# Kernel tuning notes

Measured on AMD Instinct MI355X. Metric: run time of the kernel, lower is better.

## Reference

```python
import jax, jax.numpy as jnp
import numpy as np

NLAT, NLON = 64, 64
CIN = 512
HEADS = 8


def _cc_weights(n):
    # Clenshaw-Curtis quadrature weights on [-1, 1] for nodes cos(k*pi/(n-1)),
    # as used by torch-harmonics for the 'equiangular' grid. Weights sum to 2.
    N = n - 1
    theta = np.pi * np.arange(n) / N
    m = N // 2
    j = np.arange(1, m + 1)
    b = np.where(2 * j == N, 1.0, 2.0)
    S = (b / (4.0 * j ** 2 - 1.0))[None, :] * np.cos(2.0 * j[None, :] * theta[:, None])
    w = 1.0 - S.sum(axis=1)
    c = np.full(n, 2.0)
    c[0] = 1.0
    c[-1] = 1.0
    return c * w / N


def _log_quad_weights(nlat, nlon):
    # _precompute_latitudes flips nodes/weights; then 2*pi*w/nlon tiled over lon.
    w = _cc_weights(nlat)[::-1].copy()
    qw = 2.0 * np.pi * w / nlon                       # (nlat,)
    qw = np.tile(qw[:, None], (1, nlon)).reshape(-1)  # (nlat*nlon,)
    return jnp.asarray(np.log(qw), dtype=jnp.float32)


def setup_inputs() -> dict:
    key = jax.random.key(0)
    ks = jax.random.split(key, 5)
    s_qkv = float(np.sqrt(3.0 / CIN))   # scale for q/k/v 1x1-conv weights
    s_proj = float(np.sqrt(3.0 / CIN))  # out_channels == CIN
    u = lambda k, sh, s: jax.random.uniform(k, sh, jnp.float32, -s, s)
    return dict(
        query=jax.random.normal(ks[0], (1, CIN, NLAT, NLON), jnp.float32),
        q_w=u(ks[1], (CIN, CIN), s_qkv), q_b=jnp.zeros((CIN,), jnp.float32),
        k_w=u(ks[2], (CIN, CIN), s_qkv), k_b=jnp.zeros((CIN,), jnp.float32),
        v_w=u(ks[3], (CIN, CIN), s_qkv), v_b=jnp.zeros((CIN,), jnp.float32),
        p_w=u(ks[4], (CIN, CIN), s_proj), p_b=jnp.zeros((CIN,), jnp.float32),
        log_quad_weights=_log_quad_weights(NLAT, NLON),
    )


def reference(query, q_w, q_b, k_w, k_b, v_w, v_b, p_w, p_b, log_quad_weights):
    B, C, H, W = query.shape
    hd = C // HEADS  # head dim (k_channels == out_channels == in_channels)

    def proj_tokens(x, w, b):
        # 1x1 conv == channel matmul, then split heads and flatten H*W tokens
        y = jnp.einsum('bihw,oi->bohw', x, w) + b[None, :, None, None]
        return y.reshape(B, HEADS, -1, H, W).transpose(0, 1, 3, 4, 2).reshape(B, HEADS, H * W, -1)

    q = proj_tokens(query, q_w, q_b)  # (B, heads, HW, hd)
    k = proj_tokens(query, k_w, k_b)  # self-attention: key/value default to query
    v = proj_tokens(query, v_w, v_b)

    scale = 1.0 / jnp.sqrt(jnp.asarray(hd, dtype=q.dtype))
    # additive log-quadrature bias over keys (broadcast over batch/head/query)
    logits = jnp.einsum('bhqd,bhkd->bhqk', q, k) * scale + log_quad_weights[None, None, None, :]
    attn = jax.nn.softmax(logits, axis=-1)
    out = jnp.einsum('bhqk,bhkd->bhqd', attn, v)          # (B, heads, HW, hd)
    out = out.transpose(0, 1, 3, 2).reshape(B, HEADS * hd, H, W)
    return jnp.einsum('bihw,oi->bohw', out, p_w) + p_b[None, :, None, None]
```

## Files before the change

### kernel.cpp

```cpp
#include <hip/hip_runtime.h>

typedef unsigned short u16;
typedef unsigned int u32;
typedef __bf16 bf16x8 __attribute__((ext_vector_type(8)));
typedef float f32x4 __attribute__((ext_vector_type(4)));
typedef unsigned short u16x4 __attribute__((ext_vector_type(4)));

#define LOG2E 1.4426950408889634f

#if __has_builtin(__builtin_amdgcn_exp2f)
#define EXP2F(x) __builtin_amdgcn_exp2f(x)
#else
#define EXP2F(x) exp2f(x)
#endif

__device__ __forceinline__ u16 f2bf(float f) {
    union { float f; u32 u; } a; a.f = f;
    u32 u = a.u;
    u += 0x7FFFu + ((u >> 16) & 1u);
    return (u16)(u >> 16);
}
__device__ __forceinline__ bf16x8 ldg8(const u16* p) {
    return *reinterpret_cast<const bf16x8*>(p);
}
#if __has_builtin(__builtin_amdgcn_cvt_pk_bf16_f32)
__device__ __forceinline__ u32 pack2(float a, float b) {
    auto r = __builtin_amdgcn_cvt_pk_bf16_f32(a, b);
    return __builtin_bit_cast(u32, r);
}
#else
__device__ __forceinline__ u32 pack2(float a, float b) {
    u32 ua = __float_as_uint(a) + 0x8000u;
    u32 ub = __float_as_uint(b) + 0x8000u;
    return __builtin_amdgcn_perm(ub, ua, 0x07060302);
}
#endif
__device__ __forceinline__ void async16(const void* g, void* l) {
    __builtin_amdgcn_global_load_lds(
        (const __attribute__((address_space(1))) u32*)g,
        (__attribute__((address_space(3))) u32*)l, 16, 0, 0);
}

#define MFMA16(a, b, c) __builtin_amdgcn_mfma_f32_16x16x32_bf16((a), (b), (c), 0, 0, 0)

__global__ __launch_bounds__(256) void prep(const float* __restrict__ X,
                                            u16* __restrict__ Xt,
                                            const float* __restrict__ s0,
                                            const float* __restrict__ s1,
                                            const float* __restrict__ s2,
                                            const float* __restrict__ s3,
                                            u16* __restrict__ Wqkv,
                                            u16* __restrict__ Wp,
                                            const float* __restrict__ lqw,
                                            float* __restrict__ lqw2g) {
    __shared__ u16 tile[64][65];
    const int tid = threadIdx.x;
    const int y = blockIdx.y;

    if (y < 8) {
        const int t0 = blockIdx.x * 64;
        const int c0 = y * 64;
#pragma unroll
        for (int i = 0; i < 16; ++i) {
            int idx = tid + i * 256;
            int r = idx >> 6, cc = idx & 63;
            tile[r][cc] = f2bf(X[(size_t)(c0 + r) * 4096 + t0 + cc]);
        }
        __syncthreads();
#pragma unroll
        for (int i = 0; i < 16; ++i) {
            int idx = tid + i * 256;
            int tr = idx >> 6, cc = idx & 63;
            Xt[(size_t)(t0 + tr) * 512 + c0 + cc] = tile[cc][tr];
        }
    } else if (y < 12) {
        const int m = y - 8;
        const float* s = (m == 0) ? s0 : (m == 1) ? s1 : (m == 2) ? s2 : s3;
        u16* d = (m == 3) ? Wp : Wqkv + (size_t)m * 262144;
#pragma unroll
        for (int j = 0; j < 4; ++j) {
            int i = blockIdx.x * 1024 + j * 256 + tid;
            float4 v = reinterpret_cast<const float4*>(s)[i];
            u16x4 o;
            o[0] = f2bf(v.x); o[1] = f2bf(v.y); o[2] = f2bf(v.z); o[3] = f2bf(v.w);
            reinterpret_cast<u16x4*>(d)[i] = o;
        }
    } else {
        if (blockIdx.x < 4) {
            int i = blockIdx.x * 256 + tid;
            float4 v = reinterpret_cast<const float4*>(lqw)[i];
            v.x *= LOG2E; v.y *= LOG2E; v.z *= LOG2E; v.w *= LOG2E;
            reinterpret_cast<float4*>(lqw2g)[i] = v;
        }
    }
}

__global__ __launch_bounds__(512, 2) void qkv_gemm(const u16* __restrict__ Wqkv,
                                                   const u16* __restrict__ Xt,
                                                   const float* __restrict__ qb,
                                                   const float* __restrict__ kb,
                                                   const float* __restrict__ vb,
                                                   u16* __restrict__ Qt,
                                                   u16* __restrict__ Kt,
                                                   u16* __restrict__ Vp) {
    __shared__ __align__(16) u16 Al[2][128 * 32];
    __shared__ __align__(16) u16 Bl[2][128 * 32];

    const int tid = threadIdx.x;
    const int w = tid >> 6, lane = tid & 63;
    const int quad = lane >> 4, lm = lane & 15;
    const int wm = w & 1, wn = w >> 1;
    const int n0 = blockIdx.x * 128;
    const int my = blockIdx.y;
    const int m0 = my * 128;

    const int arow = lane >> 2;
    const int sch = (lane & 3) ^ ((lane >> 3) & 3);
    const u16* agp = Wqkv + (size_t)(m0 + w * 16 + arow) * 512 + sch * 8;
    const u16* bgp = Xt + (size_t)(n0 + w * 16 + arow) * 512 + sch * 8;

    async16(agp, &Al[0][w * 16 * 32]);
    async16(bgp, &Bl[0][w * 16 * 32]);
    agp += 32; bgp += 32;

    const int FOFF = lm * 64 + ((quad ^ ((lm >> 1) & 3)) << 4);

    f32x4 acc[4][2];
#pragma unroll
    for (int mt = 0; mt < 4; ++mt)
#pragma unroll
        for (int bt = 0; bt < 2; ++bt) acc[mt][bt] = (f32x4){0.f, 0.f, 0.f, 0.f};

    __syncthreads();

    for (int s = 0; s < 16; ++s) {
        const int buf = s & 1;
        if (s < 15) {
            async16(agp, &Al[buf ^ 1][w * 16 * 32]);
            async16(bgp, &Bl[buf ^ 1][w * 16 * 32]);
            agp += 32; bgp += 32;
        }
        const char* Ab = (const char*)&Al[buf][0];
        const char* Bb = (const char*)&Bl[buf][0];
        bf16x8 af[4], bfr[2];
#pragma unroll
        for (int mt = 0; mt < 4; ++mt)
            af[mt] = *(const bf16x8*)(Ab + wm * 4096 + mt * 1024 + FOFF);
#pragma unroll
        for (int bt = 0; bt < 2; ++bt)
            bfr[bt] = *(const bf16x8*)(Bb + wn * 2048 + bt * 1024 + FOFF);
#pragma unroll
        for (int mt = 0; mt < 4; ++mt)
#pragma unroll
            for (int bt = 0; bt < 2; ++bt)
                acc[mt][bt] = MFMA16(af[mt], bfr[bt], acc[mt][bt]);
        __syncthreads();
    }

    const int mat = my >> 2;
    const float* bias = (mat == 0) ? qb : (mat == 1) ? kb : vb;
    const int chbase = (my & 3) * 128 + wm * 64 + quad * 4;

    if (mat < 2) {
        u16* out = mat ? Kt : Qt;
        const float sc = mat ? 1.0f : 0.125f * LOG2E;
#pragma unroll
        for (int mt = 0; mt < 4; ++mt) {
            const int ch = chbase + mt * 16;
            float4 bv = *(const float4*)(bias + ch);
            float bvf[4] = {bv.x, bv.y, bv.z, bv.w};
#pragma unroll
            for (int bt = 0; bt < 2; ++bt) {
                int tok = n0 + wn * 32 + bt * 16 + lm;
                u16x4 pk;
#pragma unroll
                for (int r = 0; r < 4; ++r)
                    pk[r] = f2bf((acc[mt][bt][r] + bvf[r]) * sc);
                *(u16x4*)(out + (size_t)tok * 512 + ch) = pk;
            }
        }
    } else {
#pragma unroll
        for (int mt = 0; mt < 4; ++mt) {
            const int ch = chbase + mt * 16;
            float4 bv = *(const float4*)(bias + ch);
            float bvf[4] = {bv.x, bv.y, bv.z, bv.w};
#pragma unroll
            for (int bt = 0; bt < 2; ++bt) {
                int g = bt * 16 + lm;
                int col = n0 + wn * 32 + 8 * ((g >> 2) & 3) + 4 * ((g >> 4) & 1) + (g & 3);
#pragma unroll
                for (int r = 0; r < 4; ++r)
                    Vp[(size_t)(ch + r) * 4096 + col] = f2bf(acc[mt][bt][r] + bvf[r]);
            }
        }
    }
}

__global__ __launch_bounds__(256, 2) void out_gemm(const u16* __restrict__ Wp,
                                                   const u16* __restrict__ Ot,
                                                   const float* __restrict__ pb,
                                                   float* __restrict__ out) {
    __shared__ __align__(16) u16 Al[2][128 * 32];
    __shared__ __align__(16) u16 Bl[2][64 * 32];

    const int tid = threadIdx.x;
    const int w = tid >> 6, lane = tid & 63;
    const int quad = lane >> 4, lm = lane & 15;
    const int wm = w & 1, wn = w >> 1;
    const int n0 = blockIdx.x * 64;
    const int m0 = blockIdx.y * 128;

    const int arow = lane >> 2;
    const int sch = (lane & 3) ^ ((lane >> 3) & 3);
    const u16* agp0 = Wp + (size_t)(m0 + w * 16 + arow) * 512 + sch * 8;
    const u16* agp1 = agp0 + (size_t)64 * 512;
    const u16* bgp = Ot + (size_t)(n0 + w * 16 + arow) * 512 + sch * 8;

    async16(agp0, &Al[0][w * 16 * 32]);
    async16(agp1, &Al[0][(64 + w * 16) * 32]);
    async16(bgp, &Bl[0][w * 16 * 32]);
    agp0 += 32; agp1 += 32; bgp += 32;

    const int FOFF = lm * 64 + ((quad ^ ((lm >> 1) & 3)) << 4);

    f32x4 acc[4][2];
#pragma unroll
    for (int mt = 0; mt < 4; ++mt)
#pragma unroll
        for (int bt = 0; bt < 2; ++bt) acc[mt][bt] = (f32x4){0.f, 0.f, 0.f, 0.f};

    __syncthreads();

    for (int s = 0; s < 16; ++s) {
        const int buf = s & 1;
        if (s < 15) {
            async16(agp0, &Al[buf ^ 1][w * 16 * 32]);
            async16(agp1, &Al[buf ^ 1][(64 + w * 16) * 32]);
            async16(bgp, &Bl[buf ^ 1][w * 16 * 32]);
            agp0 += 32; agp1 += 32; bgp += 32;
        }
        const char* Ab = (const char*)&Al[buf][0];
        const char* Bb = (const char*)&Bl[buf][0];
        bf16x8 af[4], bfr[2];
#pragma unroll
        for (int mt = 0; mt < 4; ++mt)
            af[mt] = *(const bf16x8*)(Ab + wm * 4096 + mt * 1024 + FOFF);
#pragma unroll
        for (int bt = 0; bt < 2; ++bt)
            bfr[bt] = *(const bf16x8*)(Bb + wn * 2048 + bt * 1024 + FOFF);
#pragma unroll
        for (int mt = 0; mt < 4; ++mt)
#pragma unroll
            for (int bt = 0; bt < 2; ++bt)
                acc[mt][bt] = MFMA16(af[mt], bfr[bt], acc[mt][bt]);
        __syncthreads();
    }

#pragma unroll
    for (int mt = 0; mt < 4; ++mt) {
        const int ch = m0 + wm * 64 + mt * 16 + quad * 4;
        float4 bv = *(const float4*)(pb + ch);
        float bvf[4] = {bv.x, bv.y, bv.z, bv.w};
#pragma unroll
        for (int bt = 0; bt < 2; ++bt) {
            int tok = n0 + wn * 32 + bt * 16 + lm;
#pragma unroll
            for (int r = 0; r < 4; ++r)
                out[(size_t)(ch + r) * 4096 + tok] = acc[mt][bt][r] + bvf[r];
        }
    }
}

__global__ __launch_bounds__(512, 2) void flash_attn(const u16* __restrict__ Qt,
                                                     const u16* __restrict__ Kt,
                                                     const u16* __restrict__ Vp,
                                                     const float* __restrict__ lqw2g,
                                                     u16* __restrict__ Ot) {
    __shared__ __align__(16) u16 kv[2][2][2][4096];

    const int tid = threadIdx.x;
    const int w = tid >> 6, lane = tid & 63;
    const int quad = lane >> 4, lm = lane & 15;
    const int qw = w & 3, half = w >> 2;
    const int h = blockIdx.y, hq = h * 64;
    const int q0 = blockIdx.x * 64 + qw * 16;
    const int kstart = half * 2048;

    char* kvb = (char*)&kv[0][0][0][0] + half * 32768;
    const int srow = lane >> 3;
    const int schunk = (lane & 7) ^ srow;
    const u16* kgp = Kt + (size_t)(kstart + qw * 16 + srow) * 512 + hq + schunk * 8;
    const u16* kgp8 = kgp + (size_t)8 * 512;
    const u16* vgp = Vp + (size_t)(hq + qw * 16 + srow) * 4096 + kstart + schunk * 8;
    const u16* vgp8 = vgp + (size_t)8 * 4096;

    {
        char* nb = kvb + qw * 2048;
        async16(kgp, nb);        async16(kgp8, nb + 1024);
        async16(vgp, nb + 8192); async16(vgp8, nb + 8192 + 1024);
        kgp += 64 * 512; kgp8 += 64 * 512; vgp += 64; vgp8 += 64;
    }

    const int A0 = lm * 128 + (((quad ^ (lm & 3)) + 4 * ((lm >> 2) & 1)) << 4);
    const int A1 = A0 ^ 64;

    const u16* qbase = Qt + (size_t)(q0 + lm) * 512 + hq + quad * 8;
    const bf16x8 bq0 = ldg8(qbase);
    const bf16x8 bq1 = ldg8(qbase + 32);

    union { u32 u[4]; bf16x8 v; } onesu;
    onesu.u[0] = onesu.u[1] = onesu.u[2] = onesu.u[3] = 0x3F803F80u;
    const bf16x8 onesv = onesu.v;

    f32x4 acc_o[4];
#pragma unroll
    for (int mt = 0; mt < 4; ++mt) acc_o[mt] = (f32x4){0.f, 0.f, 0.f, 0.f};
    f32x4 acc_l = (f32x4){0.f, 0.f, 0.f, 0.f};

    __syncthreads();

#define ATTN_STEP(BUF, KT0, DO_STAGE)                                          \
    {                                                                          \
        if (DO_STAGE) {                                                        \
            char* nb = kvb + (((BUF) ^ 1) * 16384) + qw * 2048;                \
            async16(kgp, nb);        async16(kgp8, nb + 1024);                 \
            async16(vgp, nb + 8192); async16(vgp8, nb + 8192 + 1024);          \
            kgp += 64 * 512; kgp8 += 64 * 512; vgp += 64; vgp8 += 64;          \
        }                                                                      \
        const char* Kb = kvb + (BUF) * 16384;                                  \
        u32 pk[4][2];                                                          \
        _Pragma("unroll")                                                      \
        for (int nt = 0; nt < 4; ++nt) {                                       \
            bf16x8 k0 = *(const bf16x8*)(Kb + nt * 2048 + A0);                 \
            bf16x8 k1 = *(const bf16x8*)(Kb + nt * 2048 + A1);                 \
            f32x4 a = *(const f32x4*)(lqw2g + (KT0) + nt * 16 + quad * 4);     \
            a = MFMA16(k0, bq0, a);                                            \
            a = MFMA16(k1, bq1, a);                                            \
            float p0 = EXP2F(a[0]);                                            \
            float p1 = EXP2F(a[1]);                                            \
            float p2 = EXP2F(a[2]);                                            \
            float p3 = EXP2F(a[3]);                                            \
            pk[nt][0] = pack2(p0, p1);                                         \
            pk[nt][1] = pack2(p2, p3);                                         \
        }                                                                      \
        const char* Vb = kvb + (BUF) * 16384 + 8192;                           \
        _Pragma("unroll")                                                      \
        for (int kc = 0; kc < 2; ++kc) {                                       \
            union { u32 u[4]; bf16x8 v; } bb;                                  \
            bb.u[0] = pk[2 * kc][0];                                           \
            bb.u[1] = pk[2 * kc][1];                                           \
            bb.u[2] = pk[2 * kc + 1][0];                                       \
            bb.u[3] = pk[2 * kc + 1][1];                                       \
            const int Ax = kc ? A1 : A0;                                       \
            _Pragma("unroll")                                                  \
            for (int mt = 0; mt < 4; ++mt) {                                   \
                bf16x8 vv = *(const bf16x8*)(Vb + mt * 2048 + Ax);             \
                acc_o[mt] = MFMA16(vv, bb.v, acc_o[mt]);                       \
            }                                                                  \
            acc_l = MFMA16(onesv, bb.v, acc_l);                                \
        }                                                                      \
        __syncthreads();                                                       \
    }

    for (int kt0 = kstart; kt0 < kstart + 2048; kt0 += 128) {
        ATTN_STEP(0, kt0, true)
        ATTN_STEP(1, kt0 + 64, (kt0 + 128 < kstart + 2048))
    }
#undef ATTN_STEP

    float* mbuf = (float*)&kv[0][0][0][0];
    if (half == 1) {
        float* ob = mbuf + qw * 1024;
#pragma unroll
        for (int mt = 0; mt < 4; ++mt)
            *(f32x4*)(ob + lm * 64 + mt * 16 + quad * 4) = acc_o[mt];
        if (quad == 0) mbuf[4096 + qw * 16 + lm] = acc_l[0];
    }
    __syncthreads();
    if (half == 1) return;

    float* ob = mbuf + qw * 1024;
    float inv = 1.0f / (acc_l[0] + mbuf[4096 + qw * 16 + lm]);
#pragma unroll
    for (int mt = 0; mt < 4; ++mt) {
        f32x4 o1 = *(const f32x4*)(ob + lm * 64 + mt * 16 + quad * 4);
        u16x4 pkv;
#pragma unroll
        for (int r = 0; r < 4; ++r)
            pkv[r] = f2bf((acc_o[mt][r] + o1[r]) * inv);
        *reinterpret_cast<u16x4*>(Ot + (size_t)(q0 + lm) * 512 + hq + mt * 16 + quad * 4) = pkv;
    }
}

extern "C" void kernel_launch(void* const* d_in, const int* in_sizes, int n_in,
                              void* d_out, int out_size, void* d_ws, size_t ws_size,
                              hipStream_t stream) {
    (void)in_sizes; (void)n_in; (void)out_size; (void)ws_size;
    const float* X   = (const float*)d_in[0];
    const float* qw  = (const float*)d_in[1];
    const float* qb  = (const float*)d_in[2];
    const float* kw  = (const float*)d_in[3];
    const float* kb  = (const float*)d_in[4];
    const float* vw  = (const float*)d_in[5];
    const float* vb  = (const float*)d_in[6];
    const float* pw  = (const float*)d_in[7];
    const float* pb  = (const float*)d_in[8];
    const float* lqw = (const float*)d_in[9];

    const size_t E = (size_t)4096 * 512;
    const size_t WE = (size_t)512 * 512;
    u16* Xt    = (u16*)d_ws;
    u16* Qt    = Xt + E;
    u16* Kt    = Qt + E;
    u16* Vp    = Kt + E;
    u16* Wqkv  = Vp + E;
    u16* Wp    = Wqkv + 3 * WE;
    float* lqw2g = (float*)(Wp + WE);
    u16* Ot    = Xt;

    prep<<<dim3(64, 13), dim3(256), 0, stream>>>(X, Xt, qw, kw, vw, pw,
                                                 Wqkv, Wp, lqw, lqw2g);
    qkv_gemm<<<dim3(32, 12), dim3(512), 0, stream>>>(Wqkv, Xt, qb, kb, vb, Qt, Kt, Vp);
    flash_attn<<<dim3(64, 8), dim3(512), 0, stream>>>(Qt, Kt, Vp, lqw2g, Ot);
    out_gemm<<<dim3(64, 4), dim3(256), 0, stream>>>(Wp, Ot, pb, (float*)d_out);
}
```

Baseline: 84.72 us.

## Split flash attention keys four ways with two query tiles per wave

Each wave now processes 32 queries (two 16-row tiles) against a quarter of the keys, reusing every K and V fragment loaded from LDS for both query tiles. The shared K/V staging buffer shrinks to 32-key steps per quarter, and launch bounds allow four blocks per CU instead of two. The partial outputs and row sums from the three non-leading quarters are reduced through LDS. This cuts LDS traffic per MFMA and aims for higher occupancy, at the cost of more accumulator registers, more barrier steps and a larger final reduction.

```diff
diff --git a/kernel.cpp b/kernel.cpp
--- a/kernel.cpp
+++ b/kernel.cpp
@@ -272,124 +272,154 @@
     }
 }
 
-__global__ __launch_bounds__(512, 2) void flash_attn(const u16* __restrict__ Qt,
+__global__ __launch_bounds__(512, 4) void flash_attn(const u16* __restrict__ Qt,
                                                      const u16* __restrict__ Kt,
                                                      const u16* __restrict__ Vp,
                                                      const float* __restrict__ lqw2g,
                                                      u16* __restrict__ Ot) {
-    __shared__ __align__(16) u16 kv[2][2][2][4096];
+    __shared__ __align__(16) u16 kv[4][2][2][2048];
 
     const int tid = threadIdx.x;
     const int w = tid >> 6, lane = tid & 63;
     const int quad = lane >> 4, lm = lane & 15;
-    const int qw = w & 3, half = w >> 2;
+    const int qg = w & 1, quarter = w >> 1;
     const int h = blockIdx.y, hq = h * 64;
-    const int q0 = blockIdx.x * 64 + qw * 16;
-    const int kstart = half * 2048;
-
-    char* kvb = (char*)&kv[0][0][0][0] + half * 32768;
+    const int q0 = blockIdx.x * 64 + qg * 32;
+    const int kstart = quarter * 1024;
+
+    char* kvb = (char*)&kv[0][0][0][0] + quarter * 16384;
+
     const int srow = lane >> 3;
     const int schunk = (lane & 7) ^ srow;
-    const u16* kgp = Kt + (size_t)(kstart + qw * 16 + srow) * 512 + hq + schunk * 8;
+    const u16* kgp = Kt + (size_t)(kstart + qg * 16 + srow) * 512 + hq + schunk * 8;
     const u16* kgp8 = kgp + (size_t)8 * 512;
-    const u16* vgp = Vp + (size_t)(hq + qw * 16 + srow) * 4096 + kstart + schunk * 8;
-    const u16* vgp8 = vgp + (size_t)8 * 4096;
+    const int dloc0 = qg * 32 + 2 * srow + (schunk >> 2);
+    const u16* vgpA = Vp + (size_t)(hq + dloc0) * 4096 + kstart + (schunk & 3) * 8;
+    const u16* vgpB = vgpA + (size_t)16 * 4096;
 
     {
-        char* nb = kvb + qw * 2048;
-        async16(kgp, nb);        async16(kgp8, nb + 1024);
-        async16(vgp, nb + 8192); async16(vgp8, nb + 8192 + 1024);
-        kgp += 64 * 512; kgp8 += 64 * 512; vgp += 64; vgp8 += 64;
-    }
-
-    const int A0 = lm * 128 + (((quad ^ (lm & 3)) + 4 * ((lm >> 2) & 1)) << 4);
+        char* nb = kvb;
+        async16(kgp, nb + qg * 2048);
+        async16(kgp8, nb + qg * 2048 + 1024);
+        async16(vgpA, nb + 4096 + qg * 2048);
+        async16(vgpB, nb + 4096 + qg * 2048 + 1024);
+        kgp += 32 * 512; kgp8 += 32 * 512; vgpA += 32; vgpB += 32;
+    }
+
+    const int A0 = lm * 128 + ((quad ^ (lm & 7)) << 4);
     const int A1 = A0 ^ 64;
+    const int AV = (lm >> 1) * 128 +
+                   ((((4 * (lm & 1) + quad)) ^ ((lm >> 1) & 7)) << 4);
 
     const u16* qbase = Qt + (size_t)(q0 + lm) * 512 + hq + quad * 8;
-    const bf16x8 bq0 = ldg8(qbase);
-    const bf16x8 bq1 = ldg8(qbase + 32);
+    const bf16x8 bq0a = ldg8(qbase);
+    const bf16x8 bq1a = ldg8(qbase + 32);
+    const bf16x8 bq0b = ldg8(qbase + 16 * 512);
+    const bf16x8 bq1b = ldg8(qbase + 16 * 512 + 32);
 
     union { u32 u[4]; bf16x8 v; } onesu;
     onesu.u[0] = onesu.u[1] = onesu.u[2] = onesu.u[3] = 0x3F803F80u;
     const bf16x8 onesv = onesu.v;
 
-    f32x4 acc_o[4];
-#pragma unroll
-    for (int mt = 0; mt < 4; ++mt) acc_o[mt] = (f32x4){0.f, 0.f, 0.f, 0.f};
-    f32x4 acc_l = (f32x4){0.f, 0.f, 0.f, 0.f};
+    f32x4 acc_o[4][2];
+#pragma unroll
+    for (int mt = 0; mt < 4; ++mt) {
+        acc_o[mt][0] = (f32x4){0.f, 0.f, 0.f, 0.f};
+        acc_o[mt][1] = (f32x4){0.f, 0.f, 0.f, 0.f};
+    }
+    f32x4 acc_l[2];
+    acc_l[0] = (f32x4){0.f, 0.f, 0.f, 0.f};
+    acc_l[1] = (f32x4){0.f, 0.f, 0.f, 0.f};
 
     __syncthreads();
 
 #define ATTN_STEP(BUF, KT0, DO_STAGE)                                          \
     {                                                                          \
         if (DO_STAGE) {                                                        \
-            char* nb = kvb + (((BUF) ^ 1) * 16384) + qw * 2048;                \
-            async16(kgp, nb);        async16(kgp8, nb + 1024);                 \
-            async16(vgp, nb + 8192); async16(vgp8, nb + 8192 + 1024);          \
-            kgp += 64 * 512; kgp8 += 64 * 512; vgp += 64; vgp8 += 64;          \
+            char* nb = kvb + (((BUF) ^ 1) * 8192);                             \
+            async16(kgp, nb + qg * 2048);                                      \
+            async16(kgp8, nb + qg * 2048 + 1024);                              \
+            async16(vgpA, nb + 4096 + qg * 2048);                              \
+            async16(vgpB, nb + 4096 + qg * 2048 + 1024);                       \
+            kgp += 32 * 512; kgp8 += 32 * 512; vgpA += 32; vgpB += 32;         \
         }                                                                      \
-        const char* Kb = kvb + (BUF) * 16384;                                  \
-        u32 pk[4][2];                                                          \
+        const char* Kb = kvb + (BUF) * 8192;                                   \
+        const char* Vb = Kb + 4096;                                            \
+        u32 pk[2][2][2];                                                       \
         _Pragma("unroll")                                                      \
-        for (int nt = 0; nt < 4; ++nt) {                                       \
+        for (int nt = 0; nt < 2; ++nt) {                                       \
             bf16x8 k0 = *(const bf16x8*)(Kb + nt * 2048 + A0);                 \
             bf16x8 k1 = *(const bf16x8*)(Kb + nt * 2048 + A1);                 \
-            f32x4 a = *(const f32x4*)(lqw2g + (KT0) + nt * 16 + quad * 4);     \
-            a = MFMA16(k0, bq0, a);                                            \
-            a = MFMA16(k1, bq1, a);                                            \
-            float p0 = EXP2F(a[0]);                                            \
-            float p1 = EXP2F(a[1]);                                            \
-            float p2 = EXP2F(a[2]);                                            \
-            float p3 = EXP2F(a[3]);                                            \
-            pk[nt][0] = pack2(p0, p1);                                         \
-            pk[nt][1] = pack2(p2, p3);                                         \
+            f32x4 bias = *(const f32x4*)(lqw2g + (KT0) + nt * 16 + quad * 4);  \
+            f32x4 a0 = MFMA16(k0, bq0a, bias);                                 \
+            a0 = MFMA16(k1, bq1a, a0);                                         \
+            f32x4 a1 = MFMA16(k0, bq0b, bias);                                 \
+            a1 = MFMA16(k1, bq1b, a1);                                         \
+            pk[nt][0][0] = pack2(EXP2F(a0[0]), EXP2F(a0[1]));                  \
+            pk[nt][0][1] = pack2(EXP2F(a0[2]), EXP2F(a0[3]));                  \
+            pk[nt][1][0] = pack2(EXP2F(a1[0]), EXP2F(a1[1]));                  \
+            pk[nt][1][1] = pack2(EXP2F(a1[2]), EXP2F(a1[3]));                  \
         }                                                                      \
-        const char* Vb = kvb + (BUF) * 16384 + 8192;                           \
+        union { u32 u[4]; bf16x8 v; } bb0, bb1;                                \
+        bb0.u[0] = pk[0][0][0]; bb0.u[1] = pk[0][0][1];                        \
+        bb0.u[2] = pk[1][0][0]; bb0.u[3] = pk[1][0][1];                        \
+        bb1.u[0] = pk[0][1][0]; bb1.u[1] = pk[0][1][1];                        \
+        bb1.u[2] = pk[1][1][0]; bb1.u[3] = pk[1][1][1];                        \
         _Pragma("unroll")                                                      \
-        for (int kc = 0; kc < 2; ++kc) {                                       \
-            union { u32 u[4]; bf16x8 v; } bb;                                  \
-            bb.u[0] = pk[2 * kc][0];                                           \
-            bb.u[1] = pk[2 * kc][1];                                           \
-            bb.u[2] = pk[2 * kc + 1][0];                                       \
-            bb.u[3] = pk[2 * kc + 1][1];                                       \
-            const int Ax = kc ? A1 : A0;                                       \
-            _Pragma("unroll")                                                  \
-            for (int mt = 0; mt < 4; ++mt) {                                   \
-                bf16x8 vv = *(const bf16x8*)(Vb + mt * 2048 + Ax);             \
-                acc_o[mt] = MFMA16(vv, bb.v, acc_o[mt]);                       \
-            }                                                                  \
-            acc_l = MFMA16(onesv, bb.v, acc_l);                                \
+        for (int mt = 0; mt < 4; ++mt) {                                       \
+            bf16x8 vv = *(const bf16x8*)(Vb + mt * 1024 + AV);                 \
+            acc_o[mt][0] = MFMA16(vv, bb0.v, acc_o[mt][0]);                    \
+            acc_o[mt][1] = MFMA16(vv, bb1.v, acc_o[mt][1]);                    \
         }                                                                      \
+        acc_l[0] = MFMA16(onesv, bb0.v, acc_l[0]);                             \
+        acc_l[1] = MFMA16(onesv, bb1.v, acc_l[1]);                             \
         __syncthreads();                                                       \
     }
 
-    for (int kt0 = kstart; kt0 < kstart + 2048; kt0 += 128) {
+    for (int kt0 = kstart; kt0 < kstart + 1024; kt0 += 64) {
         ATTN_STEP(0, kt0, true)
-        ATTN_STEP(1, kt0 + 64, (kt0 + 128 < kstart + 2048))
+        ATTN_STEP(1, kt0 + 32, (kt0 + 64 < kstart + 1024))
     }
 #undef ATTN_STEP
 
     float* mbuf = (float*)&kv[0][0][0][0];
-    if (half == 1) {
-        float* ob = mbuf + qw * 1024;
-#pragma unroll
-        for (int mt = 0; mt < 4; ++mt)
-            *(f32x4*)(ob + lm * 64 + mt * 16 + quad * 4) = acc_o[mt];
-        if (quad == 0) mbuf[4096 + qw * 16 + lm] = acc_l[0];
+    if (quarter != 0) {
+        const int widx = (quarter - 1) * 2 + qg;
+        float* ob = mbuf + widx * 2048;
+#pragma unroll
+        for (int s = 0; s < 2; ++s)
+#pragma unroll
+            for (int mt = 0; mt < 4; ++mt)
+                *(f32x4*)(ob + (s * 16 + lm) * 64 + mt * 16 + quad * 4) = acc_o[mt][s];
+        if (quad == 0) {
+            mbuf[12288 + widx * 32 + lm] = acc_l[0][0];
+            mbuf[12288 + widx * 32 + 16 + lm] = acc_l[1][0];
+        }
     }
     __syncthreads();
-    if (half == 1) return;
-
-    float* ob = mbuf + qw * 1024;
-    float inv = 1.0f / (acc_l[0] + mbuf[4096 + qw * 16 + lm]);
-#pragma unroll
-    for (int mt = 0; mt < 4; ++mt) {
-        f32x4 o1 = *(const f32x4*)(ob + lm * 64 + mt * 16 + quad * 4);
-        u16x4 pkv;
-#pragma unroll
-        for (int r = 0; r < 4; ++r)
-            pkv[r] = f2bf((acc_o[mt][r] + o1[r]) * inv);
-        *reinterpret_cast<u16x4*>(Ot + (size_t)(q0 + lm) * 512 + hq + mt * 16 + quad * 4) = pkv;
+    if (quarter != 0) return;
+
+#pragma unroll
+    for (int s = 0; s < 2; ++s) {
+        float lsum = acc_l[s][0];
+#pragma unroll
+        for (int p = 0; p < 3; ++p)
+            lsum += mbuf[12288 + (p * 2 + qg) * 32 + s * 16 + lm];
+        const float inv = 1.0f / lsum;
+#pragma unroll
+        for (int mt = 0; mt < 4; ++mt) {
+            f32x4 o = acc_o[mt][s];
+#pragma unroll
+            for (int p = 0; p < 3; ++p)
+                o += *(const f32x4*)(mbuf + (p * 2 + qg) * 2048 +
+                                     (s * 16 + lm) * 64 + mt * 16 + quad * 4);
+            u16x4 pkv;
+#pragma unroll
+            for (int r = 0; r < 4; ++r)
+                pkv[r] = f2bf(o[r] * inv);
+            *reinterpret_cast<u16x4*>(Ot + (size_t)(q0 + s * 16 + lm) * 512 +
+                                      hq + mt * 16 + quad * 4) = pkv;
+        }
     }
 }
 
```

Result: slower. 86.85 us (+2.5%).
